# Optimization experiments

Measured on AMD Instinct MI355X. Metric: run time of the kernel, lower is better.

The kernel has to match this reference:

```python
import jax, jax.numpy as jnp
import numpy as np

NUM_FEATURES = 256
NUM_SAMPLES = 262144
BATCH = 1024
MOMENTUM = 0.1
EPS = 1e-12


def setup_inputs() -> dict:
    key = jax.random.key(0)
    k_in, k_tgt, k_feat = jax.random.split(key, 3)
    inputs = jax.random.normal(k_in, (BATCH, NUM_FEATURES), dtype=jnp.float32)
    targets = jax.random.randint(k_tgt, (BATCH,), 0, NUM_SAMPLES, dtype=jnp.int64)
    # memory bank buffer: init as L2-normalized random rows (post-warmup state;
    # the module registers it as zeros but it is populated during training)
    feats = jax.random.normal(k_feat, (NUM_SAMPLES, NUM_FEATURES), dtype=jnp.float32)
    feats = feats / jnp.maximum(jnp.linalg.norm(feats, axis=-1, keepdims=True), EPS)
    return {"inputs": inputs, "targets": targets, "features": feats}


def reference(inputs, targets, features):
    """Sequential momentum update of the memory bank (Euclidean branch).

    Faithful to the Python loop: duplicate targets are applied in order, each
    update seeing the result of the previous ones. lax.scan carries the table.
    """
    m = jnp.float32(MOMENTUM)

    def step(feats, xy):
        x, y = xy  # x: [F], y: scalar int
        updated = m * feats[y] + (1.0 - m) * x
        updated = updated / jnp.maximum(jnp.linalg.norm(updated), EPS)
        return feats.at[y].set(updated), None

    feats, _ = jax.lax.scan(step, features, (inputs, targets))
    return feats
```

## Files before the change

kernel.cpp:

```cpp
#include <hip/hip_runtime.h>

#define NUM_FEATURES 256
#define NUM_SAMPLES  262144
#define BATCH        1024

typedef float f4 __attribute__((ext_vector_type(4)));

#define COPY_BLOCKS 2048
#define COPY_THREADS 256

__global__ __launch_bounds__(COPY_THREADS) void table_copy(
    const f4* __restrict__ src, f4* __restrict__ dst, long n4)
{
    const long tid = (long)blockIdx.x * COPY_THREADS + threadIdx.x;
    const long T = (long)COPY_BLOCKS * COPY_THREADS;
    for (long i = tid; i < n4; i += 2 * T) {
        f4 v0 = __builtin_nontemporal_load(&src[i]);
        f4 v1 = __builtin_nontemporal_load(&src[i + T]);
        dst[i] = v0;
        dst[i + T] = v1;
    }
}

__global__ __launch_bounds__(64) void memory_bank_update(
    const float* __restrict__ inputs,
    const int*   __restrict__ targets,
    const float* __restrict__ features,
    float*       __restrict__ out)
{
    __shared__ int t[BATCH];
    const int lane = threadIdx.x;
    const int b = blockIdx.x;

    const int4* tg4 = reinterpret_cast<const int4*>(targets);
    int4* t4 = reinterpret_cast<int4*>(t);
    #pragma unroll
    for (int k = 0; k < BATCH / 4 / 64; ++k)
        t4[k * 64 + lane] = tg4[k * 64 + lane];
    __syncthreads();

    const int y = t[b];

    for (int base = 0; base < b; base += 64) {
        const int j = base + lane;
        if (__any(j < b && t[j] == y)) return;
    }

    f4 v = reinterpret_cast<const f4*>(features + (size_t)y * NUM_FEATURES)[lane];

    const float m  = 0.1f;
    const float om = 1.0f - m;

    for (int base = b & ~63; base < BATCH; base += 64) {
        const int i = base + lane;
        unsigned long long mask = __ballot(i >= b && t[i] == y);
        while (mask) {
            const int i0 = base + (__ffsll((long long)mask) - 1);
            mask &= mask - 1;

            f4 x = reinterpret_cast<const f4*>(
                       inputs + (size_t)i0 * NUM_FEATURES)[lane];
            v.x = m * v.x + om * x.x;
            v.y = m * v.y + om * x.y;
            v.z = m * v.z + om * x.z;
            v.w = m * v.w + om * x.w;

            float s = v.x * v.x + v.y * v.y + v.z * v.z + v.w * v.w;
            #pragma unroll
            for (int off = 32; off > 0; off >>= 1)
                s += __shfl_xor(s, off);

            const float inv = 1.0f / fmaxf(sqrtf(s), 1e-12f);
            v.x *= inv; v.y *= inv; v.z *= inv; v.w *= inv;
        }
    }

    reinterpret_cast<f4*>(out + (size_t)y * NUM_FEATURES)[lane] = v;
}

extern "C" void kernel_launch(void* const* d_in, const int* in_sizes, int n_in,
                              void* d_out, int out_size, void* d_ws, size_t ws_size,
                              hipStream_t stream) {
    const float* inputs   = (const float*)d_in[0];
    const int*   targets  = (const int*)d_in[1];
    const float* features = (const float*)d_in[2];
    float*       out      = (float*)d_out;

    const long n4 = (long)NUM_SAMPLES * NUM_FEATURES / 4;
    table_copy<<<COPY_BLOCKS, COPY_THREADS, 0, stream>>>(
        reinterpret_cast<const f4*>(features),
        reinterpret_cast<f4*>(out), n4);

    memory_bank_update<<<BATCH, 64, 0, stream>>>(inputs, targets, features, out);
}
```

Measured before the change: 96.13 us.

## Fuse chain computation into table copy kernel and scatter results afterward

Runs the per-target momentum/normalize chain inside the first 1024 blocks of the bulk copy kernel, writing results to workspace with ownership flags. A small scatter kernel then writes owned rows into the output. This aims to overlap the latency-bound chain work with the bandwidth-bound copy instead of running it serially afterwards. It adds workspace traffic and an extra launch, and may delay some copy blocks.

```diff
diff --git a/kernel.cpp b/kernel.cpp
--- a/kernel.cpp
+++ b/kernel.cpp
@@ -8,6 +8,94 @@
 
 #define COPY_BLOCKS 2048
 #define COPY_THREADS 256
+
+#define WS_ROWS_BYTES ((size_t)BATCH * NUM_FEATURES * sizeof(float))
+#define WS_NEEDED     (WS_ROWS_BYTES + (size_t)BATCH * sizeof(int))
+
+__global__ __launch_bounds__(COPY_THREADS) void fused_copy_chain(
+    const float* __restrict__ inputs,
+    const int*   __restrict__ targets,
+    const float* __restrict__ features,
+    float*       __restrict__ out,
+    float*       __restrict__ ws_rows,
+    int*         __restrict__ ws_flags)
+{
+    const int b    = blockIdx.x;
+    const int wave = threadIdx.x >> 6;
+    const int lane = threadIdx.x & 63;
+
+    __shared__ int t[BATCH];
+
+    if (b < BATCH && wave == 0) {
+        const int4* tg4 = reinterpret_cast<const int4*>(targets);
+        int4* t4 = reinterpret_cast<int4*>(t);
+        #pragma unroll
+        for (int k = 0; k < BATCH / 4 / 64; ++k)
+            t4[k * 64 + lane] = tg4[k * 64 + lane];
+        const int y = t[b];
+
+        bool owner = true;
+        for (int base = 0; base < b; base += 64) {
+            const int j = base + lane;
+            if (__any(j < b && t[j] == y)) { owner = false; break; }
+        }
+
+        if (owner) {
+            f4 v = reinterpret_cast<const f4*>(
+                       features + (size_t)y * NUM_FEATURES)[lane];
+            const float m  = 0.1f;
+            const float om = 1.0f - m;
+            for (int base = b & ~63; base < BATCH; base += 64) {
+                const int i = base + lane;
+                unsigned long long mask = __ballot(i >= b && t[i] == y);
+                while (mask) {
+                    const int i0 = base + (__ffsll((long long)mask) - 1);
+                    mask &= mask - 1;
+                    f4 x = reinterpret_cast<const f4*>(
+                               inputs + (size_t)i0 * NUM_FEATURES)[lane];
+                    v.x = m * v.x + om * x.x;
+                    v.y = m * v.y + om * x.y;
+                    v.z = m * v.z + om * x.z;
+                    v.w = m * v.w + om * x.w;
+                    float s = v.x * v.x + v.y * v.y + v.z * v.z + v.w * v.w;
+                    #pragma unroll
+                    for (int off = 32; off > 0; off >>= 1)
+                        s += __shfl_xor(s, off);
+                    const float inv = 1.0f / fmaxf(sqrtf(s), 1e-12f);
+                    v.x *= inv; v.y *= inv; v.z *= inv; v.w *= inv;
+                }
+            }
+            reinterpret_cast<f4*>(ws_rows + (size_t)b * NUM_FEATURES)[lane] = v;
+        }
+        if (lane == 0) ws_flags[b] = owner ? 1 : 0;
+    }
+
+    const long gtid = (long)b * COPY_THREADS + threadIdx.x;
+    const long T  = (long)COPY_BLOCKS * COPY_THREADS;
+    const long n4 = (long)NUM_SAMPLES * NUM_FEATURES / 4;
+    const f4* src = reinterpret_cast<const f4*>(features);
+    f4* dst = reinterpret_cast<f4*>(out);
+    for (long i = gtid; i < n4; i += 2 * T) {
+        f4 v0 = __builtin_nontemporal_load(&src[i]);
+        f4 v1 = __builtin_nontemporal_load(&src[i + T]);
+        dst[i] = v0;
+        dst[i + T] = v1;
+    }
+}
+
+__global__ __launch_bounds__(64) void scatter_rows(
+    const int*   __restrict__ targets,
+    const float* __restrict__ ws_rows,
+    const int*   __restrict__ ws_flags,
+    float*       __restrict__ out)
+{
+    const int b = blockIdx.x;
+    if (!ws_flags[b]) return;
+    const int lane = threadIdx.x;
+    const int y = targets[b];
+    f4 v = reinterpret_cast<const f4*>(ws_rows + (size_t)b * NUM_FEATURES)[lane];
+    reinterpret_cast<f4*>(out + (size_t)y * NUM_FEATURES)[lane] = v;
+}
 
 __global__ __launch_bounds__(COPY_THREADS) void table_copy(
     const f4* __restrict__ src, f4* __restrict__ dst, long n4)
@@ -40,14 +128,12 @@
     __syncthreads();
 
     const int y = t[b];
-
     for (int base = 0; base < b; base += 64) {
         const int j = base + lane;
         if (__any(j < b && t[j] == y)) return;
     }
 
     f4 v = reinterpret_cast<const f4*>(features + (size_t)y * NUM_FEATURES)[lane];
-
     const float m  = 0.1f;
     const float om = 1.0f - m;
 
@@ -57,24 +143,20 @@
         while (mask) {
             const int i0 = base + (__ffsll((long long)mask) - 1);
             mask &= mask - 1;
-
             f4 x = reinterpret_cast<const f4*>(
                        inputs + (size_t)i0 * NUM_FEATURES)[lane];
             v.x = m * v.x + om * x.x;
             v.y = m * v.y + om * x.y;
             v.z = m * v.z + om * x.z;
             v.w = m * v.w + om * x.w;
-
             float s = v.x * v.x + v.y * v.y + v.z * v.z + v.w * v.w;
             #pragma unroll
             for (int off = 32; off > 0; off >>= 1)
                 s += __shfl_xor(s, off);
-
             const float inv = 1.0f / fmaxf(sqrtf(s), 1e-12f);
             v.x *= inv; v.y *= inv; v.z *= inv; v.w *= inv;
         }
     }
-
     reinterpret_cast<f4*>(out + (size_t)y * NUM_FEATURES)[lane] = v;
 }
 
@@ -85,11 +167,18 @@
     const int*   targets  = (const int*)d_in[1];
     const float* features = (const float*)d_in[2];
     float*       out      = (float*)d_out;
+    const long n4 = (long)NUM_SAMPLES * NUM_FEATURES / 4;
 
-    const long n4 = (long)NUM_SAMPLES * NUM_FEATURES / 4;
-    table_copy<<<COPY_BLOCKS, COPY_THREADS, 0, stream>>>(
-        reinterpret_cast<const f4*>(features),
-        reinterpret_cast<f4*>(out), n4);
-
-    memory_bank_update<<<BATCH, 64, 0, stream>>>(inputs, targets, features, out);
+    if (ws_size >= WS_NEEDED) {
+        float* ws_rows  = (float*)d_ws;
+        int*   ws_flags = (int*)((char*)d_ws + WS_ROWS_BYTES);
+        fused_copy_chain<<<COPY_BLOCKS, COPY_THREADS, 0, stream>>>(
+            inputs, targets, features, out, ws_rows, ws_flags);
+        scatter_rows<<<BATCH, 64, 0, stream>>>(targets, ws_rows, ws_flags, out);
+    } else {
+        table_copy<<<COPY_BLOCKS, COPY_THREADS, 0, stream>>>(
+            reinterpret_cast<const f4*>(features),
+            reinterpret_cast<f4*>(out), n4);
+        memory_bank_update<<<BATCH, 64, 0, stream>>>(inputs, targets, features, out);
+    }
 }
```

Result: no change. 96.91 us (+0.8%).
